# Kernel optimization log

Hardware: AMD Instinct MI355X
Metric: run time of the kernel (lower is better)

Reference implementation:

```python
import jax, jax.numpy as jnp
from jax import lax
import numpy as np

SEQ, BATCH, IN_SIZE = 512, 256, 58
HIDDEN = 256
N_LAYERS = 2
N_CAT = 18


def setup_inputs() -> dict:
    key = jax.random.key(0)
    ks = jax.random.split(key, 12)
    s = 1.0 / np.sqrt(HIDDEN)
    u = lambda k, shape: jax.random.uniform(k, shape, jnp.float32, -s, s)
    return {
        "x": jax.random.normal(ks[0], (SEQ, BATCH, IN_SIZE), jnp.float32),
        "W_ih0": u(ks[1], (3 * HIDDEN, IN_SIZE)),
        "W_hh0": u(ks[2], (3 * HIDDEN, HIDDEN)),
        "b_ih0": u(ks[3], (3 * HIDDEN,)),
        "b_hh0": u(ks[4], (3 * HIDDEN,)),
        "W_ih1": u(ks[5], (3 * HIDDEN, HIDDEN)),
        "W_hh1": u(ks[6], (3 * HIDDEN, HIDDEN)),
        "b_ih1": u(ks[7], (3 * HIDDEN,)),
        "b_hh1": u(ks[8], (3 * HIDDEN,)),
        "fc_w": u(ks[9], (N_CAT, HIDDEN)),
        "fc_b": u(ks[10], (N_CAT,)),
    }


def gru_layer(x, W_ih, W_hh, b_ih, b_hh):
    # x: (T, B, I). PyTorch GRU gate order: r, z, n.
    H = W_hh.shape[1]
    gx = jnp.einsum('tbi,gi->tbg', x, W_ih) + b_ih  # precompute input gates (T,B,3H)

    def step(h, gx_t):
        gh = h @ W_hh.T + b_hh                      # (B, 3H)
        r = jax.nn.sigmoid(gx_t[:, :H] + gh[:, :H])
        z = jax.nn.sigmoid(gx_t[:, H:2 * H] + gh[:, H:2 * H])
        n = jnp.tanh(gx_t[:, 2 * H:] + r * gh[:, 2 * H:])
        h_new = (1.0 - z) * n + z * h
        return h_new, h_new

    h0 = jnp.zeros((x.shape[1], H), x.dtype)
    _, out = lax.scan(step, h0, gx)                 # out: (T, B, H)
    return out


def reference(x, W_ih0, W_hh0, b_ih0, b_hh0, W_ih1, W_hh1, b_ih1, b_hh1, fc_w, fc_b):
    h = gru_layer(x, W_ih0, W_hh0, b_ih0, b_hh0)
    h = gru_layer(h, W_ih1, W_hh1, b_ih1, b_hh1)
    # final linear on last timestep only: (B, H) @ (H, C) + (C,)
    return h[-1] @ fc_w.T + fc_b
```

## Files before the change

kernel.cpp:

```cpp
#include <hip/hip_runtime.h>

typedef _Float16 f16;
typedef _Float16 f16x2 __attribute__((ext_vector_type(2)));
typedef _Float16 f16x8 __attribute__((ext_vector_type(8)));
typedef float f32x4 __attribute__((ext_vector_type(4)));
typedef unsigned int u32;

#define SEQ   512
#define BATCH 256
#define INS   58
#define INP   64
#define HID   256
#define NCAT  18
#define G3    (3*HID)
#define TC    128
#define NCHUNK (SEQ/TC)
#define MC    (TC*BATCH)

__device__ __forceinline__ float fdot2f(u32 a, u32 b, float c) {
#if __has_builtin(__builtin_amdgcn_fdot2)
  return __builtin_amdgcn_fdot2(__builtin_bit_cast(f16x2, a),
                                __builtin_bit_cast(f16x2, b), c, false);
#else
  f16x2 av = __builtin_bit_cast(f16x2, a);
  f16x2 bv = __builtin_bit_cast(f16x2, b);
  return c + (float)av[0] * (float)bv[0] + (float)av[1] * (float)bv[1];
#endif
}

__global__ void k_convert_pad(const float* __restrict__ src, f16* __restrict__ dst,
                              int rows, int scols, int dcols) {
  int i = blockIdx.x * blockDim.x + threadIdx.x;
  int total = rows * dcols;
  if (i >= total) return;
  int r = i / dcols, c = i - r * dcols;
  float v = (c < scols) ? src[(size_t)r * scols + c] : 0.f;
  dst[i] = (f16)v;
}

#define BM 128
#define BN 128
#define BK 32
#define LDP 40

__global__ __launch_bounds__(256, 2)
void k_gemm_f16(const f16* __restrict__ A, const f16* __restrict__ W,
                const float* __restrict__ bias, f16* __restrict__ out,
                int K) {
  __shared__ __align__(16) f16 As[BM][LDP];
  __shared__ __align__(16) f16 Ws[BN][LDP];
  const int tid  = threadIdx.x;
  const int lane = tid & 63;
  const int wave = tid >> 6;
  const int wm = wave >> 1, wn = wave & 1;
  const int n0 = blockIdx.x * BN;
  const int m0 = blockIdx.y * BM;

  f32x4 acc[4][4] = {};

  for (int k0 = 0; k0 < K; k0 += BK) {
    __syncthreads();
#pragma unroll
    for (int c = 0; c < 2; ++c) {
      int j   = c * 256 + tid;
      int row = j >> 2;
      int kc  = j & 3;
      uint4 va = *(const uint4*)(A + (size_t)(m0 + row) * K + k0 + kc * 8);
      *(uint4*)(&As[row][kc * 8]) = va;
      uint4 vw = *(const uint4*)(W + (size_t)(n0 + row) * K + k0 + kc * 8);
      *(uint4*)(&Ws[row][kc * 8]) = vw;
    }
    __syncthreads();
    const int rsel = lane & 15;
    const int ks   = (lane >> 4) * 8;
    f16x8 af[4], bf[4];
#pragma unroll
    for (int i = 0; i < 4; ++i)
      af[i] = *(const f16x8*)(&As[wm * 64 + i * 16 + rsel][ks]);
#pragma unroll
    for (int j = 0; j < 4; ++j)
      bf[j] = *(const f16x8*)(&Ws[wn * 64 + j * 16 + rsel][ks]);
#pragma unroll
    for (int i = 0; i < 4; ++i)
#pragma unroll
      for (int j = 0; j < 4; ++j)
        acc[i][j] = __builtin_amdgcn_mfma_f32_16x16x32_f16(af[i], bf[j], acc[i][j], 0, 0, 0);
  }

#pragma unroll
  for (int j = 0; j < 4; ++j) {
    int col = n0 + wn * 64 + j * 16 + (lane & 15);
    float bv = bias[col];
#pragma unroll
    for (int i = 0; i < 4; ++i) {
      int rbase = m0 + wm * 64 + i * 16 + ((lane >> 4) << 2);
#pragma unroll
      for (int rr = 0; rr < 4; ++rr)
        out[(size_t)(rbase + rr) * G3 + col] = (f16)(acc[i][j][rr] + bv);
    }
  }
}

template <int FINAL>
__global__ __launch_bounds__(512, 2)
void k_gru(const f16* __restrict__ gx,
           const f16* __restrict__ Whh,
           const float* __restrict__ bhh,
           f16* __restrict__ hout,
           float* __restrict__ hstate,
           int first, int last,
           const float* __restrict__ fcw,
           const float* __restrict__ fcb,
           float* __restrict__ out) {
  const int b   = blockIdx.x;
  const int tid = threadIdx.x;
  const int k2  = tid >> 8;
  const int r   = tid & 255;

  __shared__ __align__(16) f16 hsh[HID];
  __shared__ float psum[G3];

  u32 w0[64], w1[64], w2[64];
  {
    const f16* base = Whh + (size_t)k2 * 128;
#pragma unroll
    for (int c = 0; c < 16; ++c) {
      uint4 v0 = *(const uint4*)(base + (size_t)(0 * HID + r) * HID + c * 8);
      w0[c * 4 + 0] = v0.x; w0[c * 4 + 1] = v0.y; w0[c * 4 + 2] = v0.z; w0[c * 4 + 3] = v0.w;
      uint4 v1 = *(const uint4*)(base + (size_t)(1 * HID + r) * HID + c * 8);
      w1[c * 4 + 0] = v1.x; w1[c * 4 + 1] = v1.y; w1[c * 4 + 2] = v1.z; w1[c * 4 + 3] = v1.w;
      uint4 v2 = *(const uint4*)(base + (size_t)(2 * HID + r) * HID + c * 8);
      w2[c * 4 + 0] = v2.x; w2[c * 4 + 1] = v2.y; w2[c * 4 + 2] = v2.z; w2[c * 4 + 3] = v2.w;
    }
  }

  float bhr = 0.f, bhz = 0.f, bhn = 0.f;
  float hprev = 0.f;
  if (k2 == 0) {
    bhr = bhh[r]; bhz = bhh[HID + r]; bhn = bhh[2 * HID + r];
    hprev = first ? 0.f : hstate[(size_t)b * HID + r];
    hsh[r] = (f16)hprev;
  }

  float gxr = 0.f, gxz = 0.f, gxn = 0.f;
  if (k2 == 0) {
    const f16* g0 = gx + ((size_t)0 * BATCH + b) * G3;
    gxr = (float)g0[r]; gxz = (float)g0[HID + r]; gxn = (float)g0[2 * HID + r];
  }
  __syncthreads();

  for (int t = 0; t < TC; ++t) {
    float nxr = 0.f, nxz = 0.f, nxn = 0.f;
    if (k2 == 0 && t + 1 < TC) {
      const f16* gn = gx + ((size_t)(t + 1) * BATCH + b) * G3;
      nxr = (float)gn[r]; nxz = (float)gn[HID + r]; nxn = (float)gn[2 * HID + r];
    }

    float ar = 0.f, az = 0.f, an = 0.f;
    const uint4* hp = (const uint4*)(hsh + k2 * 128);
#pragma unroll
    for (int c = 0; c < 16; ++c) {
      uint4 v = hp[c];
      u32 h4[4] = {v.x, v.y, v.z, v.w};
#pragma unroll
      for (int q = 0; q < 4; ++q) {
        ar = fdot2f(w0[c * 4 + q], h4[q], ar);
        az = fdot2f(w1[c * 4 + q], h4[q], az);
        an = fdot2f(w2[c * 4 + q], h4[q], an);
      }
    }

    if (k2 == 1) { psum[r] = ar; psum[HID + r] = az; psum[2 * HID + r] = an; }
    __syncthreads();

    if (k2 == 0) {
      float ghr = ar + psum[r]           + bhr;
      float ghz = az + psum[HID + r]     + bhz;
      float ghn = an + psum[2 * HID + r] + bhn;
      float rg = 1.f / (1.f + __expf(-(gxr + ghr)));
      float zg = 1.f / (1.f + __expf(-(gxz + ghz)));
      float nt = gxn + rg * ghn;
      float e2 = __expf(-2.f * fabsf(nt));
      float th = (1.f - e2) / (1.f + e2);
      float ng = (nt >= 0.f) ? th : -th;
      float hn = (1.f - zg) * ng + zg * hprev;
      hprev = hn;
      hsh[r] = (f16)hn;
      if (hout) hout[((size_t)t * BATCH + b) * HID + r] = (f16)hn;
      gxr = nxr; gxz = nxz; gxn = nxn;
    }
    __syncthreads();
  }

  if (k2 == 0) hstate[(size_t)b * HID + r] = hprev;

  if (FINAL) {
    if (last) {
      if (k2 == 0) psum[r] = hprev;
      __syncthreads();
      if (tid < NCAT) {
        float s = fcb[tid];
        for (int q = 0; q < HID; ++q) s += fcw[(size_t)tid * HID + q] * psum[q];
        out[(size_t)b * NCAT + tid] = s;
      }
    }
  }
}

extern "C" void kernel_launch(void* const* d_in, const int* in_sizes, int n_in,
                              void* d_out, int out_size, void* d_ws, size_t ws_size,
                              hipStream_t stream) {
  const float* x    = (const float*)d_in[0];
  const float* Wih0 = (const float*)d_in[1];
  const float* Whh0 = (const float*)d_in[2];
  const float* bih0 = (const float*)d_in[3];
  const float* bhh0 = (const float*)d_in[4];
  const float* Wih1 = (const float*)d_in[5];
  const float* Whh1 = (const float*)d_in[6];
  const float* bih1 = (const float*)d_in[7];
  const float* bhh1 = (const float*)d_in[8];
  const float* fcw  = (const float*)d_in[9];
  const float* fcb  = (const float*)d_in[10];
  float* out = (float*)d_out;

  char* ws = (char*)d_ws;
  size_t off = 0;
  f16*   whh0h = (f16*)(ws + off); off += (size_t)G3 * HID * 2;
  f16*   whh1h = (f16*)(ws + off); off += (size_t)G3 * HID * 2;
  f16*   wih0h = (f16*)(ws + off); off += (size_t)G3 * INP * 2;
  f16*   wih1h = (f16*)(ws + off); off += (size_t)G3 * HID * 2;
  float* h0st  = (float*)(ws + off); off += (size_t)BATCH * HID * 4;
  float* h1st  = (float*)(ws + off); off += (size_t)BATCH * HID * 4;
  f16*   xhc   = (f16*)(ws + off); off += (size_t)MC * INP * 2;
  f16*   h0c   = (f16*)(ws + off); off += (size_t)MC * HID * 2;
  f16*   gxc   = (f16*)(ws + off); off += (size_t)MC * G3 * 2;

  k_convert_pad<<<(G3 * INP + 255) / 256, 256, 0, stream>>>(Wih0, wih0h, G3, INS, INP);
  k_convert_pad<<<(G3 * HID + 255) / 256, 256, 0, stream>>>(Whh0, whh0h, G3, HID, HID);
  k_convert_pad<<<(G3 * HID + 255) / 256, 256, 0, stream>>>(Wih1, wih1h, G3, HID, HID);
  k_convert_pad<<<(G3 * HID + 255) / 256, 256, 0, stream>>>(Whh1, whh1h, G3, HID, HID);

  for (int c = 0; c < NCHUNK; ++c) {
    int first = (c == 0), last = (c == NCHUNK - 1);
    const float* xc = x + (size_t)c * MC * INS;

    k_convert_pad<<<(MC * INP + 255) / 256, 256, 0, stream>>>(xc, xhc, MC, INS, INP);
    k_gemm_f16<<<dim3(G3 / BN, MC / BM), 256, 0, stream>>>(xhc, wih0h, bih0, gxc, INP);
    k_gru<0><<<BATCH, 512, 0, stream>>>(gxc, whh0h, bhh0, h0c, h0st, first, last,
                                        nullptr, nullptr, nullptr);
    k_gemm_f16<<<dim3(G3 / BN, MC / BM), 256, 0, stream>>>(h0c, wih1h, bih1, gxc, HID);
    k_gru<1><<<BATCH, 512, 0, stream>>>(gxc, whh1h, bhh1, nullptr, h1st, first, last,
                                        fcw, fcb, out);
  }
}
```

Measured before the change: 1.470 ms.

## Pair adjacent lanes for K-split and reduce via shuffle with double-buffered hidden state

Remaps the two K-halves of each hidden row onto adjacent lanes, so partial dot products are combined with a warp shuffle instead of a shared-memory psum and an extra barrier per timestep. Double-buffers the hidden state in shared memory so only one __syncthreads per step is needed. Also parallelises the final FC dot products across 16 segments. Adjacent-lane layout now makes odd lanes idle during the gate math, and the asm constraints pin weights in VGPRs at some risk of register pressure.

Result: slower. 1.790 ms (+21.7%).

```diff
diff --git a/kernel.cpp b/kernel.cpp
--- a/kernel.cpp
+++ b/kernel.cpp
@@ -114,15 +114,16 @@
            float* __restrict__ out) {
   const int b   = blockIdx.x;
   const int tid = threadIdx.x;
-  const int k2  = tid >> 8;
-  const int r   = tid & 255;
-
-  __shared__ __align__(16) f16 hsh[HID];
-  __shared__ float psum[G3];
+  const int r   = tid >> 1;
+  const int kh  = tid & 1;
+
+  __shared__ __align__(16) f16 hsh[2][HID];
+  __shared__ float red[HID];
+  __shared__ float red2[NCAT * 16];
 
   u32 w0[64], w1[64], w2[64];
   {
-    const f16* base = Whh + (size_t)k2 * 128;
+    const f16* base = Whh + (size_t)kh * 128;
 #pragma unroll
     for (int c = 0; c < 16; ++c) {
       uint4 v0 = *(const uint4*)(base + (size_t)(0 * HID + r) * HID + c * 8);
@@ -133,50 +134,59 @@
       w2[c * 4 + 0] = v2.x; w2[c * 4 + 1] = v2.y; w2[c * 4 + 2] = v2.z; w2[c * 4 + 3] = v2.w;
     }
   }
+#pragma unroll
+  for (int i = 0; i < 64; ++i)
+    asm volatile("" : "+v"(w0[i]), "+v"(w1[i]), "+v"(w2[i]));
 
   float bhr = 0.f, bhz = 0.f, bhn = 0.f;
   float hprev = 0.f;
-  if (k2 == 0) {
+  if (kh == 0) {
     bhr = bhh[r]; bhz = bhh[HID + r]; bhn = bhh[2 * HID + r];
     hprev = first ? 0.f : hstate[(size_t)b * HID + r];
-    hsh[r] = (f16)hprev;
+    hsh[0][r] = (f16)hprev;
   }
 
   float gxr = 0.f, gxz = 0.f, gxn = 0.f;
-  if (k2 == 0) {
+  if (kh == 0) {
     const f16* g0 = gx + ((size_t)0 * BATCH + b) * G3;
     gxr = (float)g0[r]; gxz = (float)g0[HID + r]; gxn = (float)g0[2 * HID + r];
   }
   __syncthreads();
 
+  int cur = 0;
   for (int t = 0; t < TC; ++t) {
     float nxr = 0.f, nxz = 0.f, nxn = 0.f;
-    if (k2 == 0 && t + 1 < TC) {
+    if (kh == 0 && t + 1 < TC) {
       const f16* gn = gx + ((size_t)(t + 1) * BATCH + b) * G3;
       nxr = (float)gn[r]; nxz = (float)gn[HID + r]; nxn = (float)gn[2 * HID + r];
     }
 
     float ar = 0.f, az = 0.f, an = 0.f;
-    const uint4* hp = (const uint4*)(hsh + k2 * 128);
+    const uint4* hp = (const uint4*)(&hsh[cur][kh * 128]);
 #pragma unroll
     for (int c = 0; c < 16; ++c) {
       uint4 v = hp[c];
-      u32 h4[4] = {v.x, v.y, v.z, v.w};
-#pragma unroll
-      for (int q = 0; q < 4; ++q) {
-        ar = fdot2f(w0[c * 4 + q], h4[q], ar);
-        az = fdot2f(w1[c * 4 + q], h4[q], az);
-        an = fdot2f(w2[c * 4 + q], h4[q], an);
-      }
-    }
-
-    if (k2 == 1) { psum[r] = ar; psum[HID + r] = az; psum[2 * HID + r] = an; }
-    __syncthreads();
-
-    if (k2 == 0) {
-      float ghr = ar + psum[r]           + bhr;
-      float ghz = az + psum[HID + r]     + bhz;
-      float ghn = an + psum[2 * HID + r] + bhn;
+      ar = fdot2f(w0[c * 4 + 0], v.x, ar);
+      az = fdot2f(w1[c * 4 + 0], v.x, az);
+      an = fdot2f(w2[c * 4 + 0], v.x, an);
+      ar = fdot2f(w0[c * 4 + 1], v.y, ar);
+      az = fdot2f(w1[c * 4 + 1], v.y, az);
+      an = fdot2f(w2[c * 4 + 1], v.y, an);
+      ar = fdot2f(w0[c * 4 + 2], v.z, ar);
+      az = fdot2f(w1[c * 4 + 2], v.z, az);
+      an = fdot2f(w2[c * 4 + 2], v.z, an);
+      ar = fdot2f(w0[c * 4 + 3], v.w, ar);
+      az = fdot2f(w1[c * 4 + 3], v.w, az);
+      an = fdot2f(w2[c * 4 + 3], v.w, an);
+    }
+    ar += __shfl_xor(ar, 1);
+    az += __shfl_xor(az, 1);
+    an += __shfl_xor(an, 1);
+
+    if (kh == 0) {
+      float ghr = ar + bhr;
+      float ghz = az + bhz;
+      float ghn = an + bhn;
       float rg = 1.f / (1.f + __expf(-(gxr + ghr)));
       float zg = 1.f / (1.f + __expf(-(gxz + ghz)));
       float nt = gxn + rg * ghn;
@@ -185,22 +195,34 @@
       float ng = (nt >= 0.f) ? th : -th;
       float hn = (1.f - zg) * ng + zg * hprev;
       hprev = hn;
-      hsh[r] = (f16)hn;
-      if (hout) hout[((size_t)t * BATCH + b) * HID + r] = (f16)hn;
+      hsh[cur ^ 1][r] = (f16)hn;
+      if (!FINAL) hout[((size_t)t * BATCH + b) * HID + r] = (f16)hn;
       gxr = nxr; gxz = nxz; gxn = nxn;
     }
     __syncthreads();
-  }
-
-  if (k2 == 0) hstate[(size_t)b * HID + r] = hprev;
+    cur ^= 1;
+  }
+
+  if (kh == 0) hstate[(size_t)b * HID + r] = hprev;
 
   if (FINAL) {
     if (last) {
-      if (k2 == 0) psum[r] = hprev;
+      if (kh == 0) red[r] = hprev;
+      __syncthreads();
+      int c = tid >> 4, seg = tid & 15;
+      if (c < NCAT) {
+        const float* wrow = fcw + (size_t)c * HID + seg * 16;
+        const float* hseg = red + seg * 16;
+        float s = 0.f;
+#pragma unroll
+        for (int q = 0; q < 16; ++q) s += wrow[q] * hseg[q];
+        red2[c * 16 + seg] = s;
+      }
       __syncthreads();
       if (tid < NCAT) {
         float s = fcb[tid];
-        for (int q = 0; q < HID; ++q) s += fcw[(size_t)tid * HID + q] * psum[q];
+#pragma unroll
+        for (int k = 0; k < 16; ++k) s += red2[tid * 16 + k];
         out[(size_t)b * NCAT + tid] = s;
       }
     }
```
